# Optimization experiments

Measured on AMD Instinct MI355X. Metric: run time of the kernel, lower is better.

Reference implementation:

```python
import jax, jax.numpy as jnp
import numpy as np

N, E = 16384, 65536
N2, A2, E2 = 65536, 131072, 262144
N3, A3, E3 = 65536, 196608, 262144
B = 256
F_IN, NI2, NI3 = 16, 64, 64


def setup_inputs() -> dict:
    key = jax.random.key(0)
    ks = iter(jax.random.split(key, 80))
    def rn(shape, s=1.0):
        return jax.random.normal(next(ks), shape, jnp.float32) * s
    def ru(shape):
        return jax.random.uniform(next(ks), shape, dtype=jnp.float32)
    def ri(shape, hi):
        return jax.random.randint(next(ks), shape, 0, hi)
    s = 0.05
    inp = {
        "x": rn((N, F_IN)),
        "edge_index": ri((2, E), N),
        "edge_attr": ru((E, 7)),
        "batch": jnp.sort(ri((N,), B)),
        "assign2_node": ri((A2,), N),
        "assign2_cluster": ri((A2,), N2),
        "iso_type_2": ru((N2, NI2)),
        "edge_index_2": ri((2, E2), N2),
        "batch_2": jnp.sort(ri((N2,), B)),
        "assign3_node": ri((A3,), N),
        "assign3_cluster": ri((A3,), N3),
        "iso_type_3": ru((N3, NI3)),
        "edge_index_3": ri((2, E3), N3),
        "batch_3": jnp.sort(ri((N3,), B)),
    }
    for i, (mi, mo) in enumerate([(F_IN, 32), (32, 64), (64, 64)], start=1):
        inp[f"nn{i}_W1"] = rn((7, 128), s)
        inp[f"nn{i}_b1"] = jnp.zeros((128,), jnp.float32)
        inp[f"nn{i}_W2"] = rn((128, mi * mo), s)
        inp[f"nn{i}_b2"] = jnp.zeros((mi * mo,), jnp.float32)
        inp[f"conv{i}_root"] = rn((mi, mo), s)
        inp[f"conv{i}_bias"] = jnp.zeros((mo,), jnp.float32)
    for i, din in zip([4, 5, 6, 7], [64 + NI2, 64, 64 + NI3, 64]):
        inp[f"conv{i}_Wrel"] = rn((din, 64), s)
        inp[f"conv{i}_Wroot"] = rn((din, 64), s)
        inp[f"conv{i}_bias"] = jnp.zeros((64,), jnp.float32)
    inp["fc1_W"] = rn((384, 64), s); inp["fc1_b"] = jnp.zeros((64,), jnp.float32)
    inp["fc2_W"] = rn((64, 32), s); inp["fc2_b"] = jnp.zeros((32,), jnp.float32)
    inp["fc3_W"] = rn((32, 1), s); inp["fc3_b"] = jnp.zeros((1,), jnp.float32)
    return inp


def nnconv(x, ei, ea, W1, b1, W2, b2, root, bias, mi, mo):
    # edge MLP -> per-edge [mi, mo] weight matrix; message = x_src @ W_e; scatter-add to dst
    h = jax.nn.relu(ea @ W1 + b1) @ W2 + b2          # [E, mi*mo]
    We = h.reshape(-1, mi, mo)
    msg = jnp.einsum('ei,eio->eo', x[ei[0]], We)     # [E, mo]
    agg = jax.ops.segment_sum(msg, ei[1], num_segments=x.shape[0])
    return x @ root + agg + bias


def graphconv(x, ei, Wrel, Wroot, bias):
    agg = jax.ops.segment_sum(x[ei[0]], ei[1], num_segments=x.shape[0])
    return agg @ Wrel + x @ Wroot + bias


def avg_pool_assign(x, node_idx, cluster_idx, num_clusters):
    s = jax.ops.segment_sum(x[node_idx], cluster_idx, num_segments=num_clusters)
    c = jax.ops.segment_sum(jnp.ones((node_idx.shape[0],), x.dtype), cluster_idx, num_segments=num_clusters)
    return s / jnp.clip(c, 1.0)[:, None]


def reference(x, edge_index, edge_attr, batch, assign2_node, assign2_cluster, iso_type_2, edge_index_2, batch_2, assign3_node, assign3_cluster, iso_type_3, edge_index_3, batch_3, nn1_W1, nn1_b1, nn1_W2, nn1_b2, conv1_root, conv1_bias, nn2_W1, nn2_b1, nn2_W2, nn2_b2, conv2_root, conv2_bias, nn3_W1, nn3_b1, nn3_W2, nn3_b2, conv3_root, conv3_bias, conv4_Wrel, conv4_Wroot, conv4_bias, conv5_Wrel, conv5_Wroot, conv5_bias, conv6_Wrel, conv6_Wroot, conv6_bias, conv7_Wrel, conv7_Wroot, conv7_bias, fc1_W, fc1_b, fc2_W, fc2_b, fc3_W, fc3_b):
    elu = jax.nn.elu
    h = elu(nnconv(x, edge_index, edge_attr, nn1_W1, nn1_b1, nn1_W2, nn1_b2, conv1_root, conv1_bias, F_IN, 32))
    h = elu(nnconv(h, edge_index, edge_attr, nn2_W1, nn2_b1, nn2_W2, nn2_b2, conv2_root, conv2_bias, 32, 64))
    h = elu(nnconv(h, edge_index, edge_attr, nn3_W1, nn3_b1, nn3_W2, nn3_b2, conv3_root, conv3_bias, 64, 64))
    x_1 = jax.ops.segment_sum(h, batch, num_segments=B)
    # 2-set level
    h2 = avg_pool_assign(h, assign2_node, assign2_cluster, N2)
    h2 = jnp.concatenate([h2, iso_type_2], axis=1)
    h2 = elu(graphconv(h2, edge_index_2, conv4_Wrel, conv4_Wroot, conv4_bias))
    h2 = elu(graphconv(h2, edge_index_2, conv5_Wrel, conv5_Wroot, conv5_bias))
    x_2 = jax.ops.segment_sum(h2, batch_2, num_segments=B)
    # 3-set level
    h3 = avg_pool_assign(h, assign3_node, assign3_cluster, N3)
    h3 = jnp.concatenate([h3, iso_type_3], axis=1)
    h3 = elu(graphconv(h3, edge_index_3, conv6_Wrel, conv6_Wroot, conv6_bias))
    h3 = elu(graphconv(h3, edge_index_3, conv7_Wrel, conv7_Wroot, conv7_bias))
    x_3 = jax.ops.segment_sum(h3, batch_3, num_segments=B)
    xc = jnp.concatenate([x_1, x_2, x_3], axis=1)
    xc = jnp.concatenate([xc, xc], axis=1)      # [B, 384]
    o = elu(xc @ fc1_W + fc1_b)
    o = elu(o @ fc2_W + fc2_b)
    o = o @ fc3_W + fc3_b
    return o.reshape(-1)
```

## Files before the change

kernel.cpp:

```cpp
#include <hip/hip_runtime.h>
#include <math.h>

#define NN 16384
#define E1N 65536
#define NBATCH 256
#define NC2 65536
#define A2N 131072
#define A3N 196608
#define ELV 262144
#define KH 128
#define OCS 136
#define MNSTR 1092
#define ECAP 96

typedef _Float16 f16;
typedef _Float16 f16x2 __attribute__((ext_vector_type(2)));
typedef _Float16 f16x4 __attribute__((ext_vector_type(4)));
typedef _Float16 f16x8 __attribute__((ext_vector_type(8)));
typedef float    f32x4 __attribute__((ext_vector_type(4)));

__device__ __forceinline__ float elu1(float x){ return x > 0.f ? x : expm1f(x); }

__device__ __forceinline__ float dot2acc(f16x2 a, f16x2 b, float c){
#if __has_builtin(__builtin_amdgcn_fdot2)
  return __builtin_amdgcn_fdot2(a, b, c, false);
#else
  return fmaf((float)a[0], (float)b[0], fmaf((float)a[1], (float)b[1], c));
#endif
}

__global__ __launch_bounds__(256) void k_scan1(const int* __restrict__ deg,
    int* __restrict__ ptr, int* __restrict__ partials){
  __shared__ int buf[256];
  int i = blockIdx.x*256 + threadIdx.x, t = threadIdx.x;
  int v = deg[i];
  buf[t] = v; __syncthreads();
  for (int o = 1; o < 256; o <<= 1){
    int x = (t >= o) ? buf[t-o] : 0;
    __syncthreads(); buf[t] += x; __syncthreads();
  }
  ptr[i] = buf[t] - v;
  if (t == 255) partials[blockIdx.x] = buf[255];
}

__global__ __launch_bounds__(256) void k_scan2seg(int* __restrict__ partials, int nb){
  __shared__ int buf[256];
  int t = threadIdx.x, base = blockIdx.x*nb;
  int v = (t < nb) ? partials[base + t] : 0;
  buf[t] = v; __syncthreads();
  for (int o = 1; o < 256; o <<= 1){
    int x = (t >= o) ? buf[t-o] : 0;
    __syncthreads(); buf[t] += x; __syncthreads();
  }
  if (t < nb) partials[base + t] = buf[t] - v;
}

__global__ __launch_bounds__(256) void k_scan3(const int* __restrict__ partials,
    int* __restrict__ ptr, int* __restrict__ cur){
  int i = blockIdx.x*256 + threadIdx.x;
  int v = ptr[i] + partials[blockIdx.x];
  ptr[i] = v; cur[i] = v;
}

__global__ __launch_bounds__(256) void k_count_edge_dual(const int* __restrict__ ei, int* __restrict__ deg){
  int e = blockIdx.x*256 + threadIdx.x;
  if (e >= E1N) return;
  atomicAdd(&deg[ei[e]], 1);
  atomicAdd(&deg[NN + ei[E1N + e]], 1);
}

__global__ __launch_bounds__(256) void k_fill_edge_dual(const int* __restrict__ ei, int* __restrict__ cur,
    int* __restrict__ eids, int* __restrict__ srcs, int* __restrict__ dpos){
  int e = blockIdx.x*256 + threadIdx.x;
  if (e >= E1N) return;
  int s = ei[e], d = ei[E1N + e];
  int p = atomicAdd(&cur[s], 1);
  eids[p] = e; srcs[p] = s;
  int p2 = atomicAdd(&cur[NN + d], 1);
  dpos[p2] = p;
}

__global__ __launch_bounds__(256) void k_count_assign_dual(const int* __restrict__ a2c,
    const int* __restrict__ a3c, int* __restrict__ ldegA){
  int i = blockIdx.x*256 + threadIdx.x;
  if (i < A2N) atomicAdd(&ldegA[a2c[i]], 1);
  else if (i < A2N + A3N) atomicAdd(&ldegA[NC2 + a3c[i - A2N]], 1);
}

__global__ __launch_bounds__(256) void k_fill_assign_dual(const int* __restrict__ a2n,
    const int* __restrict__ a2c, const int* __restrict__ a3n, const int* __restrict__ a3c,
    int* __restrict__ curA, int* __restrict__ ans2, int* __restrict__ ans3){
  int i = blockIdx.x*256 + threadIdx.x;
  if (i < A2N){
    int p = atomicAdd(&curA[a2c[i]], 1); ans2[p] = a2n[i];
  } else if (i < A2N + A3N){
    int j = i - A2N;
    int p = atomicAdd(&curA[NC2 + a3c[j]], 1); ans3[p] = a3n[j];
  }
}

__global__ __launch_bounds__(256) void k_count_dst_dual(const int* __restrict__ ei2,
    const int* __restrict__ ei3, int* __restrict__ ldegD){
  int i = blockIdx.x*256 + threadIdx.x;
  if (i < ELV) atomicAdd(&ldegD[ei2[ELV + i]], 1);
  else if (i < 2*ELV) atomicAdd(&ldegD[NC2 + ei3[ELV + (i - ELV)]], 1);
}

__global__ __launch_bounds__(256) void k_fill_dst_dual(const int* __restrict__ ei2,
    const int* __restrict__ ei3, int* __restrict__ curD,
    int* __restrict__ dsrc2, int* __restrict__ dsrc3){
  int i = blockIdx.x*256 + threadIdx.x;
  if (i < ELV){
    int p = atomicAdd(&curD[ei2[ELV + i]], 1); dsrc2[p] = ei2[i];
  } else if (i < 2*ELV){
    int j = i - ELV;
    int p = atomicAdd(&curD[NC2 + ei3[ELV + j]], 1); dsrc3[p] = ei3[j];
  }
}

__global__ __launch_bounds__(256) void k_cvt16(const float* __restrict__ v, f16* __restrict__ o, int n){
  int t = blockIdx.x*256 + threadIdx.x;
  if (t < n) o[t] = (f16)v[t];
}

__global__ __launch_bounds__(256) void k_packPrep(const float* __restrict__ root,
    const float* __restrict__ b2, f16* __restrict__ Bp, int mi, int mo, int S, int NB){
  int t = blockIdx.x*256 + threadIdx.x;
  if (t >= NB*S*512) return;
  int j = t & 7, l = (t >> 3) & 63, cs = t >> 9;
  int s = cs % S, c = cs / S;
  int k_in = s*32 + ((l>>4)<<3) + j;
  int n = c*16 + (l & 15);
  float v = 0.f;
  if (k_in < mi) v = (n < mo) ? root[k_in*mo + n] : b2[k_in*mo + (n - mo)];
  Bp[t] = (f16)v;
}

template<int MI, int S, int NB, int MO>
__global__ __launch_bounds__(256) void k_prep_mfma(const f16* __restrict__ A,
    const f16* __restrict__ Bp, const float* __restrict__ bias,
    float* __restrict__ prep, float* __restrict__ bterm){
  int l = threadIdx.x & 63, w = threadIdx.x >> 6;
  int r0 = blockIdx.x*64 + w*16;
  const f16* arow = A + (size_t)(r0 + (l & 15))*MI;
  f16x8 a[S];
  #pragma unroll
  for (int s=0;s<S;s++){
    int koff = s*32 + ((l>>4)<<3);
    if (koff < MI) a[s] = *(const f16x8*)(arow + koff);
    else           a[s] = (f16x8){0,0,0,0,0,0,0,0};
  }
  #pragma unroll
  for (int c=0;c<NB;c++){
    f32x4 acc = (f32x4){0.f,0.f,0.f,0.f};
    #pragma unroll
    for (int s=0;s<S;s++){
      f16x8 b = *(const f16x8*)(Bp + ((size_t)(c*S + s)*64 + l)*8);
      acc = __builtin_amdgcn_mfma_f32_16x16x32_f16(a[s], b, acc, 0, 0, 0);
    }
    int col = c*16 + (l & 15);
    #pragma unroll
    for (int r=0;r<4;r++){
      int row = r0 + ((l>>4)<<2) + r;
      if (col < MO) prep[(size_t)row*MO + col] = acc[r] + bias[col];
      else          bterm[(size_t)row*MO + (col - MO)] = acc[r];
    }
  }
}

__global__ __launch_bounds__(256) void k_w2pack_full(const float* __restrict__ W2,
    f16* __restrict__ Bp, int mi, int mo, int S){
  int t = blockIdx.x*256 + threadIdx.x;
  if (t >= mo*8*S*512) return;
  int j = t & 7, l = (t >> 3) & 63, cs = t >> 9;
  int s = cs % S, q = cs / S;
  int oc = q >> 3;
  int k  = (q & 7)*16 + (l & 15);
  int i  = s*32 + ((l>>4)<<3) + j;
  float v = (i < mi) ? W2[(size_t)k*mi*mo + (size_t)i*mo + oc] : 0.f;
  Bp[t] = (f16)v;
}

template<int MI, int S, int MO>
__global__ __launch_bounds__(256) void k_nnconv_fused5(const f16* __restrict__ xin16,
    const f16* __restrict__ W2p,
    const int* __restrict__ rowptr, const int* __restrict__ rowend,
    const int* __restrict__ srcs, const int* __restrict__ eids,
    const float* __restrict__ ea, const float* __restrict__ W1,
    const float* __restrict__ b1,
    const float* __restrict__ bterm, f16* __restrict__ msg16){
  __shared__ __align__(16) f16   M[16*MNSTR];
  __shared__ __align__(16) f16   hb[ECAP*OCS];
  __shared__ __align__(16) float eas[ECAP*8];
  __shared__ float bt[16*MO];
  int t = threadIdx.x, l = t & 63, w = t >> 6;
  int n0 = blockIdx.x*16;
  int estart = rowptr[n0], eend = rowend[n0+15];
  if (estart >= eend) return;
  for (int idx = t; idx < 16*MO; idx += 256) bt[idx] = bterm[(size_t)n0*MO + idx];
  const f16* arow = xin16 + (size_t)(n0 + (l&15))*MI;
  f16x8 a[S];
  #pragma unroll
  for (int s=0;s<S;s++){
    int koff = s*32 + ((l>>4)<<3);
    if (koff < MI) a[s] = *(const f16x8*)(arow + koff);
    else           a[s] = (f16x8){0,0,0,0,0,0,0,0};
  }
  const int NCHUNK = MO/8;
  int oc = t & 7, eslot = t >> 3;
  for (int ebase = estart; ebase < eend; ebase += ECAP){
    int ecnt = eend - ebase; if (ecnt > ECAP) ecnt = ECAP;
    for (int idx = t; idx < ecnt*8; idx += 256){
      int e_ = idx >> 3, i = idx & 7;
      eas[idx] = (i < 7) ? ea[(size_t)eids[ebase + e_]*7 + i] : 0.f;
    }
    __syncthreads();
    for (int idx = t; idx < ecnt*32; idx += 256){
      int e_ = idx >> 5, p = idx & 31;
      int k0 = p*4;
      const float* xr = &eas[e_*8];
      float4 acc4 = *(const float4*)(b1 + k0);
      #pragma unroll
      for (int i=0;i<7;i++){
        float xv = xr[i];
        float4 wv = *(const float4*)(W1 + i*KH + k0);
        acc4.x = fmaf(xv, wv.x, acc4.x);
        acc4.y = fmaf(xv, wv.y, acc4.y);
        acc4.z = fmaf(xv, wv.z, acc4.z);
        acc4.w = fmaf(xv, wv.w, acc4.w);
      }
      f16x4 hv = { (f16)fmaxf(acc4.x,0.f), (f16)fmaxf(acc4.y,0.f),
                   (f16)fmaxf(acc4.z,0.f), (f16)fmaxf(acc4.w,0.f) };
      *(f16x4*)&hb[e_*OCS + k0] = hv;
    }
    __syncthreads();
    for (int c = 0; c < NCHUNK; c++){
      #pragma unroll
      for (int tt = 0; tt < 16; tt++){
        int q = c*64 + w*16 + tt;
        f32x4 acc = (f32x4){0.f,0.f,0.f,0.f};
        #pragma unroll
        for (int s=0;s<S;s++){
          f16x8 b = *(const f16x8*)(W2p + ((size_t)(q*S + s)*64 + l)*8);
          acc = __builtin_amdgcn_mfma_f32_16x16x32_f16(a[s], b, acc, 0, 0, 0);
        }
        int ocl = w*2 + (tt>>3);
        int kpos = (tt&7)*16 + (l & 15);
        f16* mp = &M[ocl*OCS + kpos];
        #pragma unroll
        for (int r=0;r<4;r++)
          mp[(size_t)(((l>>4)<<2) + r)*MNSTR] = (f16)acc[r];
      }
      __syncthreads();
      #pragma unroll
      for (int r2 = 0; r2 < ECAP/32; r2++){
        int ee = r2*32 + eslot;
        if (ee < ecnt){
          int e = ebase + ee;
          int s_ = srcs[e];
          int ln = s_ - n0;
          float acc = bt[ln*MO + c*8 + oc];
          const f16* mrow = &M[(size_t)ln*MNSTR + oc*OCS];
          const f16* hrow = &hb[ee*OCS];
          #pragma unroll 4
          for (int kk=0; kk<16; kk++){
            f16x8 h8 = *(const f16x8*)(hrow + kk*8);
            f16x4 m0 = *(const f16x4*)(mrow + kk*8);
            f16x4 m1 = *(const f16x4*)(mrow + kk*8 + 4);
            acc = dot2acc((f16x2){h8[0],h8[1]}, (f16x2){m0[0],m0[1]}, acc);
            acc = dot2acc((f16x2){h8[2],h8[3]}, (f16x2){m0[2],m0[3]}, acc);
            acc = dot2acc((f16x2){h8[4],h8[5]}, (f16x2){m1[0],m1[1]}, acc);
            acc = dot2acc((f16x2){h8[6],h8[7]}, (f16x2){m1[2],m1[3]}, acc);
          }
          msg16[(size_t)e*MO + c*8 + oc] = (f16)acc;
        }
      }
      __syncthreads();
    }
  }
}

template<int MO>
__global__ __launch_bounds__(256) void k_msg_gather(const int* __restrict__ dptr,
    const int* __restrict__ dend, const int* __restrict__ dpos,
    const f16* __restrict__ msg, const float* __restrict__ prep,
    f16* __restrict__ out16){
  int t = threadIdx.x, l = t & 63, w = t >> 6;
  int n, o;
  if (MO == 64){ n = blockIdx.x*4 + w; o = l; }
  else         { n = blockIdx.x*8 + w*2 + (l>>5); o = l & 31; }
  int st = dptr[n], en = dend[n];
  float acc = prep[(size_t)n*MO + o];
  int p = st;
  for (; p + 4 <= en; p += 4){
    int q0 = dpos[p], q1 = dpos[p+1], q2 = dpos[p+2], q3 = dpos[p+3];
    float v0 = (float)msg[(size_t)q0*MO + o];
    float v1 = (float)msg[(size_t)q1*MO + o];
    float v2 = (float)msg[(size_t)q2*MO + o];
    float v3 = (float)msg[(size_t)q3*MO + o];
    acc += (v0 + v1) + (v2 + v3);
  }
  for (; p < en; p++) acc += (float)msg[(size_t)dpos[p]*MO + o];
  out16[(size_t)n*MO + o] = (f16)elu1(acc);
}

__global__ __launch_bounds__(256) void k_pool_gather_dual(const int* __restrict__ aptr,
    const int* __restrict__ aend, const int* __restrict__ ans2, const int* __restrict__ ans3,
    const f16* __restrict__ h, const float* __restrict__ iso2, const float* __restrict__ iso3,
    f16* __restrict__ h16){
  int l = threadIdx.x & 63, w = threadIdx.x >> 6;
  int cg = blockIdx.x*4 + w;
  int lvl = cg >= NC2;
  int c = cg - lvl*NC2;
  const int* ans = lvl ? ans3 : ans2;
  const float* iso = lvl ? iso3 : iso2;
  int st = aptr[cg], en = aend[cg];
  float acc = 0.f;
  int e = st;
  for (; e + 4 <= en; e += 4){
    int n0 = ans[e], n1 = ans[e+1], n2 = ans[e+2], n3 = ans[e+3];
    float v0 = (float)h[(size_t)n0*64 + l];
    float v1 = (float)h[(size_t)n1*64 + l];
    float v2 = (float)h[(size_t)n2*64 + l];
    float v3 = (float)h[(size_t)n3*64 + l];
    acc += (v0 + v1) + (v2 + v3);
  }
  for (; e < en; e++) acc += (float)h[(size_t)ans[e]*64 + l];
  int cnt = en - st;
  float val = (cnt > 0) ? acc / (float)cnt : 0.f;
  h16[(size_t)cg*128 + l] = (f16)val;
  h16[(size_t)cg*128 + 64 + l] = (f16)iso[(size_t)c*64 + l];
}

#define BP_O4 0
#define BP_O5 16384
#define BP_O6 24576
#define BP_O7 40960
__global__ __launch_bounds__(256) void k_packB_all(
    const float* __restrict__ W4r, const float* __restrict__ W4o,
    const float* __restrict__ W5r, const float* __restrict__ W5o,
    const float* __restrict__ W6r, const float* __restrict__ W6o,
    const float* __restrict__ W7r, const float* __restrict__ W7o,
    f16* __restrict__ Bp){
  int t = blockIdx.x*256 + threadIdx.x;
  const float *Wrel, *Wroot; int S, base;
  if      (t < BP_O5){ Wrel=W4r; Wroot=W4o; S=4; base=BP_O4; }
  else if (t < BP_O6){ Wrel=W5r; Wroot=W5o; S=2; base=BP_O5; }
  else if (t < BP_O7){ Wrel=W6r; Wroot=W6o; S=4; base=BP_O6; }
  else if (t < 49152){ Wrel=W7r; Wroot=W7o; S=2; base=BP_O7; }
  else return;
  int u = t - base;
  int j = u & 7, l = (u >> 3) & 63, cs = u >> 9;
  int s = cs % S, c = cs / S;
  int k = s*32 + ((l>>4)<<3) + j;
  int n = (c<<4) + (l & 15);
  float v = (n < 64) ? Wrel[k*64 + n] : Wroot[k*64 + (n - 64)];
  Bp[t] = (f16)v;
}

template<int S>
__global__ __launch_bounds__(256) void k_gc_mfma_dual(const f16* __restrict__ Abase,
    const f16* __restrict__ Bp, int bpo2, int bpo3,
    const float* __restrict__ bias2, const float* __restrict__ bias3,
    f16* __restrict__ y16, f16* __restrict__ rbuf16){
  const int half = NC2/64;
  int lvl = blockIdx.x >= half;
  int bloc = blockIdx.x - lvl*half;
  const f16* A = Abase + (size_t)lvl*NC2*(S*32);
  const f16* B = Bp + (lvl ? bpo3 : bpo2);
  const float* bias = lvl ? bias3 : bias2;
  f16* y  = y16 + (size_t)lvl*NC2*64;
  f16* rb = rbuf16 + (size_t)lvl*NC2*64;
  int l = threadIdx.x & 63, w = threadIdx.x >> 6;
  int r0 = bloc*64 + w*16;
  const f16* arow = A + (size_t)(r0 + (l & 15))*(S*32);
  f16x8 a[S];
  #pragma unroll
  for (int s=0;s<S;s++) a[s] = *(const f16x8*)(arow + s*32 + ((l>>4)<<3));
  f32x4 acc[8];
  #pragma unroll
  for (int c=0;c<8;c++) acc[c] = (f32x4){0.f,0.f,0.f,0.f};
  #pragma unroll
  for (int c=0;c<8;c++){
    #pragma unroll
    for (int s=0;s<S;s++){
      f16x8 b = *(const f16x8*)(B + ((size_t)(c*S + s)*64 + l)*8);
      acc[c] = __builtin_amdgcn_mfma_f32_16x16x32_f16(a[s], b, acc[c], 0, 0, 0);
    }
  }
  #pragma unroll
  for (int c=0;c<8;c++){
    int col = c*16 + (l & 15);
    #pragma unroll
    for (int r=0;r<4;r++){
      int row = r0 + ((l>>4)<<2) + r;
      if (col < 64) y[(size_t)row*64 + col] = (f16)acc[c][r];
      else          rb[(size_t)row*64 + (col-64)] = (f16)(acc[c][r] + bias[col-64]);
    }
  }
}

__global__ __launch_bounds__(256) void k_gc_gather_dual(const int* __restrict__ dptrD,
    const int* __restrict__ dcurD, const int* __restrict__ dsrc2, const int* __restrict__ dsrc3,
    const f16* __restrict__ y16, const f16* __restrict__ rbuf16,
    f16* __restrict__ obase){
  int l = threadIdx.x & 63, w = threadIdx.x >> 6;
  int ng = blockIdx.x*4 + w;
  int lvl = ng >= NC2;
  int n = ng - lvl*NC2;
  const int* dsrc = lvl ? dsrc3 : dsrc2;
  const f16* y  = y16 + (size_t)lvl*NC2*64;
  const f16* rb = rbuf16 + (size_t)lvl*NC2*64;
  f16* o = obase + (size_t)lvl*NC2*64;
  int st = dptrD[ng], en = dcurD[ng];
  float acc = (float)rb[(size_t)n*64 + l];
  int e = st;
  for (; e + 4 <= en; e += 4){
    int s0 = dsrc[e], s1 = dsrc[e+1], s2 = dsrc[e+2], s3 = dsrc[e+3];
    float v0 = (float)y[(size_t)s0*64 + l];
    float v1 = (float)y[(size_t)s1*64 + l];
    float v2 = (float)y[(size_t)s2*64 + l];
    float v3 = (float)y[(size_t)s3*64 + l];
    acc += (v0 + v1) + (v2 + v3);
  }
  for (; e < en; e++) acc += (float)y[(size_t)dsrc[e]*64 + l];
  o[(size_t)n*64 + l] = (f16)elu1(acc);
}

__device__ __forceinline__ int lowerb(const int* __restrict__ a, int n, int key){
  int lo = 0, hi = n;
  while (lo < hi){ int m = (lo + hi) >> 1; if (a[m] < key) lo = m + 1; else hi = m; }
  return lo;
}

__global__ __launch_bounds__(256) void k_batchsum3(const int* __restrict__ b1,
    const int* __restrict__ b2, const int* __restrict__ b3,
    const f16* __restrict__ s1, const f16* __restrict__ s2, const f16* __restrict__ s3,
    float* __restrict__ x123){
  __shared__ float red[4][64];
  int seg = blockIdx.x >> 8, b = blockIdx.x & 255;
  const int* batch = (seg==0) ? b1 : ((seg==1) ? b2 : b3);
  const f16* src   = (seg==0) ? s1 : ((seg==1) ? s2 : s3);
  int nn = (seg==0) ? NN : NC2;
  int lo = lowerb(batch, nn, b);
  int hi = lowerb(batch, nn, b+1);
  int col = threadIdx.x & 63, wq = threadIdx.x >> 6;
  float acc = 0.f;
  for (int n = lo + wq; n < hi; n += 4) acc += (float)src[(size_t)n*64 + col];
  red[wq][col] = acc;
  __syncthreads();
  if (threadIdx.x < 64){
    float s = red[0][threadIdx.x] + red[1][threadIdx.x] + red[2][threadIdx.x] + red[3][threadIdx.x];
    x123[b*192 + seg*64 + threadIdx.x] = s;
  }
}

__global__ __launch_bounds__(256) void k_fc1(const float* __restrict__ x123,
    const float* __restrict__ W, const float* __restrict__ b, float* __restrict__ t1){
  int t = blockIdx.x*256 + threadIdx.x;
  if (t >= NBATCH*64) return;
  int bb = t >> 6, o = t & 63;
  const float* xr = x123 + bb*192;
  float acc = b[o];
  for (int j=0;j<192;j++) acc = fmaf(xr[j], W[j*64+o] + W[(192+j)*64+o], acc);
  t1[t] = elu1(acc);
}

__global__ __launch_bounds__(256) void k_fc2(const float* __restrict__ t1,
    const float* __restrict__ W, const float* __restrict__ b, float* __restrict__ t2){
  int t = blockIdx.x*256 + threadIdx.x;
  if (t >= NBATCH*32) return;
  int bb = t >> 5, o = t & 31;
  float acc = b[o];
  for (int j=0;j<64;j++) acc = fmaf(t1[bb*64+j], W[j*32+o], acc);
  t2[t] = elu1(acc);
}

__global__ __launch_bounds__(256) void k_fc3(const float* __restrict__ t2,
    const float* __restrict__ W, const float* __restrict__ b, float* __restrict__ out){
  int t = blockIdx.x*256 + threadIdx.x;
  if (t >= NBATCH) return;
  float acc = b[0];
  for (int j=0;j<32;j++) acc = fmaf(t2[t*32+j], W[j], acc);
  out[t] = acc;
}

static inline int cdiv(long long a, int b){ return (int)((a + b - 1) / b); }

extern "C" void kernel_launch(void* const* d_in, const int* in_sizes, int n_in,
                              void* d_out, int out_size, void* d_ws, size_t ws_size,
                              hipStream_t stream) {
  const float* x0    = (const float*)d_in[0];
  const int*   ei    = (const int*)d_in[1];
  const float* ea    = (const float*)d_in[2];
  const int*   batch = (const int*)d_in[3];
  const int*   a2n   = (const int*)d_in[4];
  const int*   a2c   = (const int*)d_in[5];
  const float* iso2  = (const float*)d_in[6];
  const int*   ei2   = (const int*)d_in[7];
  const int*   b2arr = (const int*)d_in[8];
  const int*   a3n   = (const int*)d_in[9];
  const int*   a3c   = (const int*)d_in[10];
  const float* iso3  = (const float*)d_in[11];
  const int*   ei3   = (const int*)d_in[12];
  const int*   b3arr = (const int*)d_in[13];
  const float* nnp[3][6];
  for (int c=0;c<3;c++) for (int p=0;p<6;p++) nnp[c][p] = (const float*)d_in[14 + 6*c + p];
  const float* c4W[3]; const float* c5W[3]; const float* c6W[3]; const float* c7W[3];
  for (int p=0;p<3;p++){ c4W[p]=(const float*)d_in[32+p]; c5W[p]=(const float*)d_in[35+p];
                         c6W[p]=(const float*)d_in[38+p]; c7W[p]=(const float*)d_in[41+p]; }
  const float* fc1W=(const float*)d_in[44]; const float* fc1b=(const float*)d_in[45];
  const float* fc2W=(const float*)d_in[46]; const float* fc2b=(const float*)d_in[47];
  const float* fc3W=(const float*)d_in[48]; const float* fc3b=(const float*)d_in[49];
  float* outp = (float*)d_out;

  char* ws = (char*)d_ws; size_t off = 0;
  auto alloc = [&](size_t bytes)->void*{ void* p = ws + off; off += (bytes + 255) & ~(size_t)255; return p; };
  const size_t SZ_R0 = (size_t)92*1024*1024;
  char* r0 = (char*)alloc(SZ_R0);
  f16*   W2p   = (f16*)r0;
  f16*   prepB = (f16*)(r0 + 2*1024*1024);
  float* bterm = (float*)(r0 + 2*1024*1024 + 64*1024);
  float* prep  = (float*)(r0 + 2*1024*1024 + 64*1024 + (size_t)NN*64*4);
  f16*   msg16 = (f16*)  (r0 + 2*1024*1024 + 64*1024 + (size_t)NN*64*8);
  size_t o2 = 0;
  auto a2 = [&](size_t bytes)->char*{ char* p = r0 + o2; o2 += (bytes + 255) & ~(size_t)255; return p; };
  f16*   h16   = (f16*)  a2((size_t)2*NC2*128*2);
  f16*   y16   = (f16*)  a2((size_t)2*NC2*64*2);
  f16*   rbuf16= (f16*)  a2((size_t)2*NC2*64*2);
  f16*   g16   = (f16*)  a2((size_t)2*NC2*64*2);
  f16*   BpGc  = (f16*)  a2((size_t)49152*2);
  int*   ldegA = (int*)  a2((size_t)4*NC2*4);
  int*   ldegD = ldegA + 2*NC2;
  int*   ptrA  = (int*)  a2((size_t)2*NC2*4);
  int*   curA  = (int*)  a2((size_t)2*NC2*4);
  int*   ptrD  = (int*)  a2((size_t)2*NC2*4);
  int*   curD  = (int*)  a2((size_t)2*NC2*4);
  int*   ans2  = (int*)  a2((size_t)A2N*4);
  int*   ans3  = (int*)  a2((size_t)A3N*4);
  int*   dsrc2 = (int*)  a2((size_t)ELV*4);
  int*   dsrc3 = (int*)  a2((size_t)ELV*4);
  f16*   fin2  = h16;
  f16*   fin3  = h16 + (size_t)NC2*64;
  f16*   x016  = (f16*)  alloc((size_t)NN*16*2);
  f16*   hA16  = (f16*)  alloc((size_t)NN*32*2);
  f16*   hB16  = (f16*)  alloc((size_t)NN*64*2);
  f16*   hC16  = (f16*)  alloc((size_t)NN*64*2);
  int*   deg1  = (int*)  alloc((size_t)2*NN*4);
  int*   ptr1  = (int*)  alloc((size_t)2*NN*4);
  int*   cur1  = (int*)  alloc((size_t)2*NN*4);
  int*   eids  = (int*)  alloc((size_t)E1N*4);
  int*   srcs  = (int*)  alloc((size_t)E1N*4);
  int*   dpos  = (int*)  alloc((size_t)E1N*4);
  int*   parts = (int*)  alloc((size_t)512*4);
  float* x123  = (float*)alloc((size_t)NBATCH*192*4);
  float* t1    = (float*)alloc((size_t)NBATCH*64*4);
  float* t2    = (float*)alloc((size_t)NBATCH*32*4);
  (void)ws_size; (void)n_in; (void)in_sizes; (void)out_size;

  auto scan = [&](const int* dg, int totalN, int segs, int* ptr, int* cur){
    int nb = totalN/256/segs;
    k_scan1<<<totalN/256,256,0,stream>>>(dg, ptr, parts);
    k_scan2seg<<<segs,256,0,stream>>>(parts, nb);
    k_scan3<<<totalN/256,256,0,stream>>>(parts, ptr, cur);
  };

  hipMemsetAsync(deg1, 0, (size_t)2*NN*4, stream);
  k_count_edge_dual<<<cdiv(E1N,256),256,0,stream>>>(ei, deg1);
  scan(deg1, 2*NN, 2, ptr1, cur1);
  k_fill_edge_dual<<<cdiv(E1N,256),256,0,stream>>>(ei, cur1, eids, srcs, dpos);
  k_cvt16<<<cdiv((long long)NN*16,256),256,0,stream>>>(x0, x016, NN*16);

  auto run_nnconv = [&](const f16* xin16, int mi, int mo,
                        const float* const* P, f16* out16){
    const float* W1=P[0]; const float* b1=P[1]; const float* W2=P[2];
    const float* b2=P[3]; const float* root=P[4]; const float* bias=P[5];
    const int S = (mi > 32) ? 2 : 1;
    const int NB = (2*mo)/16;
    k_packPrep<<<cdiv((long long)NB*S*512,256),256,0,stream>>>(root, b2, prepB, mi, mo, S, NB);
    if (mi==16)      k_prep_mfma<16,1,4,32><<<NN/64,256,0,stream>>>(xin16, prepB, bias, prep, bterm);
    else if (mi==32) k_prep_mfma<32,1,8,64><<<NN/64,256,0,stream>>>(xin16, prepB, bias, prep, bterm);
    else             k_prep_mfma<64,2,8,64><<<NN/64,256,0,stream>>>(xin16, prepB, bias, prep, bterm);
    k_w2pack_full<<<cdiv((long long)mo*8*S*512,256),256,0,stream>>>(W2, W2p, mi, mo, S);
    if (mi==16)      k_nnconv_fused5<16,1,32><<<NN/16,256,0,stream>>>(xin16, W2p, ptr1, cur1, srcs, eids, ea, W1, b1, bterm, msg16);
    else if (mi==32) k_nnconv_fused5<32,1,64><<<NN/16,256,0,stream>>>(xin16, W2p, ptr1, cur1, srcs, eids, ea, W1, b1, bterm, msg16);
    else             k_nnconv_fused5<64,2,64><<<NN/16,256,0,stream>>>(xin16, W2p, ptr1, cur1, srcs, eids, ea, W1, b1, bterm, msg16);
    if (mo==32) k_msg_gather<32><<<NN/8,256,0,stream>>>(ptr1+NN, cur1+NN, dpos, msg16, prep, out16);
    else        k_msg_gather<64><<<NN/4,256,0,stream>>>(ptr1+NN, cur1+NN, dpos, msg16, prep, out16);
  };
  run_nnconv(x016, 16, 32, nnp[0], hA16);
  run_nnconv(hA16, 32, 64, nnp[1], hB16);
  run_nnconv(hB16, 64, 64, nnp[2], hC16);

  hipMemsetAsync(ldegA, 0, (size_t)4*NC2*4, stream);
  k_count_assign_dual<<<cdiv((long long)(A2N+A3N),256),256,0,stream>>>(a2c, a3c, ldegA);
  scan(ldegA, 2*NC2, 2, ptrA, curA);
  k_fill_assign_dual<<<cdiv((long long)(A2N+A3N),256),256,0,stream>>>(a2n, a2c, a3n, a3c, curA, ans2, ans3);
  k_count_dst_dual<<<cdiv((long long)2*ELV,256),256,0,stream>>>(ei2, ei3, ldegD);
  scan(ldegD, 2*NC2, 2, ptrD, curD);
  k_fill_dst_dual<<<cdiv((long long)2*ELV,256),256,0,stream>>>(ei2, ei3, curD, dsrc2, dsrc3);

  k_pool_gather_dual<<<2*NC2/4,256,0,stream>>>(ptrA, curA, ans2, ans3, hC16, iso2, iso3, h16);
  k_packB_all<<<cdiv(49152,256),256,0,stream>>>(c4W[0], c4W[1], c5W[0], c5W[1],
                                                c6W[0], c6W[1], c7W[0], c7W[1], BpGc);
  k_gc_mfma_dual<4><<<2*NC2/64,256,0,stream>>>(h16, BpGc, BP_O4, BP_O6, c4W[2], c6W[2], y16, rbuf16);
  k_gc_gather_dual<<<2*NC2/4,256,0,stream>>>(ptrD, curD, dsrc2, dsrc3, y16, rbuf16, g16);
  k_gc_mfma_dual<2><<<2*NC2/64,256,0,stream>>>(g16, BpGc, BP_O5, BP_O7, c5W[2], c7W[2], y16, rbuf16);
  k_gc_gather_dual<<<2*NC2/4,256,0,stream>>>(ptrD, curD, dsrc2, dsrc3, y16, rbuf16, fin2);

  k_batchsum3<<<3*NBATCH,256,0,stream>>>(batch, b2arr, b3arr, hC16, fin2, fin3, x123);
  k_fc1<<<cdiv((long long)NBATCH*64,256),256,0,stream>>>(x123, fc1W, fc1b, t1);
  k_fc2<<<cdiv((long long)NBATCH*32,256),256,0,stream>>>(t1, fc2W, fc2b, t2);
  k_fc3<<<cdiv(NBATCH,256),256,0,stream>>>(t2, fc3W, fc3b, outp);
}
```

Measured before the change: 737.9 us.

## Give each wavefront private LDS tiles to drop block barriers in nnconv

Restructures the fused NNConv kernel so each wavefront computes and consumes its own pair of output channels in a private LDS slice. The per-chunk block-wide __syncthreads are replaced by wave-local lgkmcnt waits, leaving one barrier per edge batch. Two half-width LDS loads of M are also merged into one 16-byte load. This relies on wavefront lockstep for the LDS hazard, and each lane now does proportionally more dot work per pass.

```diff
diff --git a/kernel.cpp b/kernel.cpp
--- a/kernel.cpp
+++ b/kernel.cpp
@@ -10,7 +10,7 @@
 #define ELV 262144
 #define KH 128
 #define OCS 136
-#define MNSTR 1092
+#define WNSTR 280
 #define ECAP 96
 
 typedef _Float16 f16;
@@ -182,14 +182,14 @@
 }
 
 template<int MI, int S, int MO>
-__global__ __launch_bounds__(256) void k_nnconv_fused5(const f16* __restrict__ xin16,
+__global__ __launch_bounds__(256) void k_nnconv_fused7(const f16* __restrict__ xin16,
     const f16* __restrict__ W2p,
     const int* __restrict__ rowptr, const int* __restrict__ rowend,
     const int* __restrict__ srcs, const int* __restrict__ eids,
     const float* __restrict__ ea, const float* __restrict__ W1,
     const float* __restrict__ b1,
     const float* __restrict__ bterm, f16* __restrict__ msg16){
-  __shared__ __align__(16) f16   M[16*MNSTR];
+  __shared__ __align__(16) f16   M[4*16*WNSTR];
   __shared__ __align__(16) f16   hb[ECAP*OCS];
   __shared__ __align__(16) float eas[ECAP*8];
   __shared__ float bt[16*MO];
@@ -206,8 +206,9 @@
     if (koff < MI) a[s] = *(const f16x8*)(arow + koff);
     else           a[s] = (f16x8){0,0,0,0,0,0,0,0};
   }
-  const int NCHUNK = MO/8;
-  int oc = t & 7, eslot = t >> 3;
+  f16* Mw = &M[w*16*WNSTR];
+  const int NCP = MO/8;
+  int eslot = l >> 1, ocl = l & 1;
   for (int ebase = estart; ebase < eend; ebase += ECAP){
     int ecnt = eend - ebase; if (ecnt > ECAP) ecnt = ECAP;
     for (int idx = t; idx < ecnt*8; idx += 256){
@@ -234,49 +235,49 @@
       *(f16x4*)&hb[e_*OCS + k0] = hv;
     }
     __syncthreads();
-    for (int c = 0; c < NCHUNK; c++){
+    for (int i = 0; i < NCP; i++){
+      int cp = w + 4*i;
       #pragma unroll
       for (int tt = 0; tt < 16; tt++){
-        int q = c*64 + w*16 + tt;
+        int q = (2*cp + (tt>>3))*8 + (tt&7);
         f32x4 acc = (f32x4){0.f,0.f,0.f,0.f};
         #pragma unroll
         for (int s=0;s<S;s++){
           f16x8 b = *(const f16x8*)(W2p + ((size_t)(q*S + s)*64 + l)*8);
           acc = __builtin_amdgcn_mfma_f32_16x16x32_f16(a[s], b, acc, 0, 0, 0);
         }
-        int ocl = w*2 + (tt>>3);
+        int od = (tt>>3)*OCS;
         int kpos = (tt&7)*16 + (l & 15);
-        f16* mp = &M[ocl*OCS + kpos];
+        f16* mp = &Mw[od + kpos];
         #pragma unroll
         for (int r=0;r<4;r++)
-          mp[(size_t)(((l>>4)<<2) + r)*MNSTR] = (f16)acc[r];
+          mp[(size_t)(((l>>4)<<2) + r)*WNSTR] = (f16)acc[r];
       }
-      __syncthreads();
+      __asm__ volatile("s_waitcnt lgkmcnt(0)" ::: "memory");
       #pragma unroll
       for (int r2 = 0; r2 < ECAP/32; r2++){
         int ee = r2*32 + eslot;
         if (ee < ecnt){
           int e = ebase + ee;
-          int s_ = srcs[e];
-          int ln = s_ - n0;
-          float acc = bt[ln*MO + c*8 + oc];
-          const f16* mrow = &M[(size_t)ln*MNSTR + oc*OCS];
+          int ln = srcs[e] - n0;
+          float acc = bt[ln*MO + 2*cp + ocl];
+          const f16* mrow = &Mw[(size_t)ln*WNSTR + ocl*OCS];
           const f16* hrow = &hb[ee*OCS];
           #pragma unroll 4
           for (int kk=0; kk<16; kk++){
             f16x8 h8 = *(const f16x8*)(hrow + kk*8);
-            f16x4 m0 = *(const f16x4*)(mrow + kk*8);
-            f16x4 m1 = *(const f16x4*)(mrow + kk*8 + 4);
-            acc = dot2acc((f16x2){h8[0],h8[1]}, (f16x2){m0[0],m0[1]}, acc);
-            acc = dot2acc((f16x2){h8[2],h8[3]}, (f16x2){m0[2],m0[3]}, acc);
-            acc = dot2acc((f16x2){h8[4],h8[5]}, (f16x2){m1[0],m1[1]}, acc);
-            acc = dot2acc((f16x2){h8[6],h8[7]}, (f16x2){m1[2],m1[3]}, acc);
+            f16x8 m8 = *(const f16x8*)(mrow + kk*8);
+            #pragma unroll
+            for (int j=0;j<4;j++){
+              acc = dot2acc((f16x2){h8[2*j],h8[2*j+1]}, (f16x2){m8[2*j],m8[2*j+1]}, acc);
+            }
           }
-          msg16[(size_t)e*MO + c*8 + oc] = (f16)acc;
+          msg16[(size_t)e*MO + 2*cp + ocl] = (f16)acc;
         }
       }
-      __syncthreads();
+      __asm__ volatile("s_waitcnt lgkmcnt(0)" ::: "memory");
     }
+    __syncthreads();
   }
 }
 
@@ -582,9 +583,9 @@
     else if (mi==32) k_prep_mfma<32,1,8,64><<<NN/64,256,0,stream>>>(xin16, prepB, bias, prep, bterm);
     else             k_prep_mfma<64,2,8,64><<<NN/64,256,0,stream>>>(xin16, prepB, bias, prep, bterm);
     k_w2pack_full<<<cdiv((long long)mo*8*S*512,256),256,0,stream>>>(W2, W2p, mi, mo, S);
-    if (mi==16)      k_nnconv_fused5<16,1,32><<<NN/16,256,0,stream>>>(xin16, W2p, ptr1, cur1, srcs, eids, ea, W1, b1, bterm, msg16);
-    else if (mi==32) k_nnconv_fused5<32,1,64><<<NN/16,256,0,stream>>>(xin16, W2p, ptr1, cur1, srcs, eids, ea, W1, b1, bterm, msg16);
-    else             k_nnconv_fused5<64,2,64><<<NN/16,256,0,stream>>>(xin16, W2p, ptr1, cur1, srcs, eids, ea, W1, b1, bterm, msg16);
+    if (mi==16)      k_nnconv_fused7<16,1,32><<<NN/16,256,0,stream>>>(xin16, W2p, ptr1, cur1, srcs, eids, ea, W1, b1, bterm, msg16);
+    else if (mi==32) k_nnconv_fused7<32,1,64><<<NN/16,256,0,stream>>>(xin16, W2p, ptr1, cur1, srcs, eids, ea, W1, b1, bterm, msg16);
+    else             k_nnconv_fused7<64,2,64><<<NN/16,256,0,stream>>>(xin16, W2p, ptr1, cur1, srcs, eids, ea, W1, b1, bterm, msg16);
     if (mo==32) k_msg_gather<32><<<NN/8,256,0,stream>>>(ptr1+NN, cur1+NN, dpos, msg16, prep, out16);
     else        k_msg_gather<64><<<NN/4,256,0,stream>>>(ptr1+NN, cur1+NN, dpos, msg16, prep, out16);
   };
```

Result: no change. 732.3 us (-0.8%).
